# Performance work log

Hardware: AMD Instinct MI355X
Metric: run time of the kernel (lower is better)

Reference implementation:

```python
import math
import jax, jax.numpy as jnp
import numpy as np

D_MODEL = 1024
HEADS = 16
D_K = D_MODEL // HEADS
BATCH = 4
SEQ = 2048


def setup_inputs() -> dict:
    key = jax.random.key(0)
    ks = jax.random.split(key, 7)
    q = jax.random.normal(ks[0], (BATCH, SEQ, D_MODEL), dtype=jnp.float32)
    k = jax.random.normal(ks[1], (BATCH, SEQ, D_MODEL), dtype=jnp.float32)
    v = jax.random.normal(ks[2], (BATCH, SEQ, D_MODEL), dtype=jnp.float32)
    # causal mask: True = masked (filled with -inf), broadcastable over batch & heads
    mask = jnp.triu(jnp.ones((SEQ, SEQ), dtype=bool), k=1)[None, None, :, :]
    s = 1.0 / math.sqrt(D_MODEL)
    Wq = jax.random.normal(ks[3], (D_MODEL, D_MODEL), dtype=jnp.float32) * s
    Wk = jax.random.normal(ks[4], (D_MODEL, D_MODEL), dtype=jnp.float32) * s
    Wv = jax.random.normal(ks[5], (D_MODEL, D_MODEL), dtype=jnp.float32) * s
    Wo = jax.random.normal(ks[6], (D_MODEL, D_MODEL), dtype=jnp.float32) * s
    return {"q": q, "k": k, "v": v, "mask": mask, "Wq": Wq, "Wk": Wk, "Wv": Wv, "Wo": Wo}


def reference(q, k, v, mask, Wq, Wk, Wv, Wo):
    B, S, _ = q.shape
    # Linear(d_model, d_model, bias=False): y = x @ W.T
    def proj(x, W):
        return (x @ W.T).reshape(B, S, HEADS, D_K).transpose(0, 2, 1, 3)  # [B,H,S,Dk]
    qh, kh, vh = proj(q, Wq), proj(k, Wk), proj(v, Wv)
    scores = jnp.einsum('bhqd,bhkd->bhqk', qh, kh) / math.sqrt(D_K)
    scores = jnp.where(mask, -jnp.inf, scores)
    attn = jax.nn.softmax(scores, axis=-1)  # dropout p=0 is identity
    ctx = jnp.einsum('bhqk,bhkd->bhqd', attn, vh)
    ctx = ctx.transpose(0, 2, 1, 3).reshape(B, S, D_MODEL)
    return ctx @ Wo.T
```

## Files before the change

kernel.cpp:

```cpp
#include <hip/hip_runtime.h>
#include <hip/hip_bf16.h>
#include <stdint.h>

#define S_LEN 2048
#define DMODEL 1024
#define HEADS 16
#define DK 64
#define LDK 72

#define QSCALE 0.18033688011112042f

typedef __attribute__((ext_vector_type(8))) short bf16x8;
typedef __attribute__((ext_vector_type(4))) float f32x4;

__device__ __forceinline__ unsigned short f2bf(float f) {
    union { float f; unsigned u; } c; c.f = f;
    unsigned u = c.u;
    u += 0x7fffu + ((u >> 16) & 1u);
    return (unsigned short)(u >> 16);
}

__device__ __forceinline__ unsigned pkbf(float a, float b) {
    union { float f; unsigned u; } ca, cb; ca.f = a; cb.f = b;
    unsigned ua = ca.u + (0x7fffu + ((ca.u >> 16) & 1u));
    unsigned ub = cb.u + (0x7fffu + ((cb.u >> 16) & 1u));
    return __builtin_amdgcn_perm(ub, ua, 0x07060302);
}

__device__ __forceinline__ void g2lds16(const unsigned short* g, unsigned short* l) {
    __builtin_amdgcn_global_load_lds((const __attribute__((address_space(1))) void*)g,
                                     (__attribute__((address_space(3))) void*)l, 16, 0, 0);
}

__global__ __launch_bounds__(256) void convert_kernel(
    const float* __restrict__ q, const float* __restrict__ k, const float* __restrict__ v,
    const float* __restrict__ Wq, const float* __restrict__ Wk, const float* __restrict__ Wv,
    const float* __restrict__ Wo,
    unsigned short* __restrict__ qbf, unsigned short* __restrict__ kbf,
    unsigned short* __restrict__ vbf, unsigned short* __restrict__ wbf)
{
    const float* src; unsigned short* dst; int n8;
    const int y = blockIdx.y;
    if (y == 0)      { src = q;  dst = qbf;           n8 = 1048576; }
    else if (y == 1) { src = k;  dst = kbf;           n8 = 1048576; }
    else if (y == 2) { src = v;  dst = vbf;           n8 = 1048576; }
    else if (y == 3) { src = Wq; dst = wbf;           n8 = 131072; }
    else if (y == 4) { src = Wk; dst = wbf + 1048576; n8 = 131072; }
    else if (y == 5) { src = Wv; dst = wbf + 2097152; n8 = 131072; }
    else             { src = Wo; dst = wbf + 3145728; n8 = 131072; }
    int i = blockIdx.x * 256 + threadIdx.x;
    if (i >= n8) return;
    float4 f0 = ((const float4*)src)[(size_t)2 * i];
    float4 f1 = ((const float4*)src)[(size_t)2 * i + 1];
    union { unsigned u[4]; uint4 v; } o;
    o.u[0] = pkbf(f0.x, f0.y); o.u[1] = pkbf(f0.z, f0.w);
    o.u[2] = pkbf(f1.x, f1.y); o.u[3] = pkbf(f1.z, f1.w);
    *(uint4*)&dst[(size_t)8 * i] = o.v;
}

__global__ __launch_bounds__(256) void proj_gemm_kernel(
    const unsigned short* __restrict__ qbf, const unsigned short* __restrict__ kbf,
    const unsigned short* __restrict__ vbf, const unsigned short* __restrict__ wbf,
    unsigned short* __restrict__ qh, unsigned short* __restrict__ kh,
    unsigned short* __restrict__ vh_t)
{
    const unsigned short* A; const unsigned short* Bm; unsigned short* Y;
    const int z = blockIdx.z;
    if (z == 0)      { A = qbf; Bm = wbf;           Y = qh;   }
    else if (z == 1) { A = kbf; Bm = wbf + 1048576; Y = kh;   }
    else             { A = vbf; Bm = wbf + 2097152; Y = vh_t; }

    __shared__ unsigned short sA[128 * 64];
    __shared__ unsigned short sB[128 * 64];

    const int t    = threadIdx.x;
    const int lane = t & 63;
    const int wid  = t >> 6;
    const int wrow = (wid >> 1) * 64;
    const int wcol = (wid & 1) * 64;
    const int m0   = blockIdx.x * 128;
    const int n0   = blockIdx.y * 128;
    const int lrow = lane & 15;
    const int quad = lane >> 4;
    const int lk   = quad * 8;

    const unsigned short* gA = A + (size_t)(m0 + wid * 32 + (lane >> 3)) * 1024 + (lane & 7) * 8;
    const unsigned short* gB = Bm + (size_t)(n0 + wid * 32 + (lane >> 3)) * 1024 + (lane & 7) * 8;
    unsigned short* lA = sA + wid * 2048;
    unsigned short* lB = sB + wid * 2048;

    f32x4 acc[4][4];
    for (int i = 0; i < 4; i++) for (int j = 0; j < 4; j++) acc[i][j] = (f32x4){0.f, 0.f, 0.f, 0.f};

    for (int kb = 0; kb < 1024; kb += 64) {
        __syncthreads();
        for (int it = 0; it < 4; ++it) {
            g2lds16(gA + (size_t)it * 8 * 1024, lA + it * 512);
            g2lds16(gB + (size_t)it * 8 * 1024, lB + it * 512);
        }
        gA += 64; gB += 64;
        __syncthreads();
        for (int kk = 0; kk < 64; kk += 32) {
            bf16x8 a[4], b[4];
            for (int i = 0; i < 4; i++) a[i] = *(const bf16x8*)&sA[(wrow + i * 16 + lrow) * 64 + kk + lk];
            for (int j = 0; j < 4; j++) b[j] = *(const bf16x8*)&sB[(wcol + j * 16 + lrow) * 64 + kk + lk];
            for (int i = 0; i < 4; i++)
                for (int j = 0; j < 4; j++)
                    acc[i][j] = __builtin_amdgcn_mfma_f32_16x16x32_bf16(a[i], b[j], acc[i][j], 0, 0, 0);
        }
    }

    const float scale = (z == 0) ? QSCALE : 1.0f;
    for (int i = 0; i < 4; i++) {
        int grow = m0 + wrow + i * 16 + quad * 4;
        for (int j = 0; j < 4; j++) {
            int gcol = n0 + wcol + j * 16 + lrow;
            int h = gcol >> 6, d = gcol & 63;
            for (int r = 0; r < 4; r++) {
                int row = grow + r;
                int b_ = row >> 11;
                int s_ = row & 2047;
                unsigned short val = f2bf(acc[i][j][r] * scale);
                if (z == 2)
                    Y[(((size_t)(b_ * HEADS + h) * DK) + d) * S_LEN + s_] = val;
                else
                    Y[(((size_t)(b_ * HEADS + h) * S_LEN) + s_) * DK + d] = val;
            }
        }
    }
}

__global__ __launch_bounds__(256) void outproj_gemm_kernel(
    const unsigned short* __restrict__ ctx, const unsigned short* __restrict__ wobf,
    float* __restrict__ out)
{
    __shared__ unsigned short sA[128 * 64];
    __shared__ unsigned short sB[128 * 64];

    const int t    = threadIdx.x;
    const int lane = t & 63;
    const int wid  = t >> 6;
    const int wrow = (wid >> 1) * 64;
    const int wcol = (wid & 1) * 64;
    const int m0   = blockIdx.x * 128;
    const int n0   = blockIdx.y * 128;
    const int lrow = lane & 15;
    const int quad = lane >> 4;
    const int lk   = quad * 8;

    const unsigned short* gA = ctx  + (size_t)(m0 + wid * 32 + (lane >> 3)) * 1024 + (lane & 7) * 8;
    const unsigned short* gB = wobf + (size_t)(n0 + wid * 32 + (lane >> 3)) * 1024 + (lane & 7) * 8;
    unsigned short* lA = sA + wid * 2048;
    unsigned short* lB = sB + wid * 2048;

    f32x4 acc[4][4];
    for (int i = 0; i < 4; i++) for (int j = 0; j < 4; j++) acc[i][j] = (f32x4){0.f, 0.f, 0.f, 0.f};

    for (int kb = 0; kb < 1024; kb += 64) {
        __syncthreads();
        for (int it = 0; it < 4; ++it) {
            g2lds16(gA + (size_t)it * 8 * 1024, lA + it * 512);
            g2lds16(gB + (size_t)it * 8 * 1024, lB + it * 512);
        }
        gA += 64; gB += 64;
        __syncthreads();
        for (int kk = 0; kk < 64; kk += 32) {
            bf16x8 a[4], b[4];
            for (int i = 0; i < 4; i++) a[i] = *(const bf16x8*)&sA[(wrow + i * 16 + lrow) * 64 + kk + lk];
            for (int j = 0; j < 4; j++) b[j] = *(const bf16x8*)&sB[(wcol + j * 16 + lrow) * 64 + kk + lk];
            for (int i = 0; i < 4; i++)
                for (int j = 0; j < 4; j++)
                    acc[i][j] = __builtin_amdgcn_mfma_f32_16x16x32_bf16(a[i], b[j], acc[i][j], 0, 0, 0);
        }
    }

    for (int i = 0; i < 4; i++) {
        int grow = m0 + wrow + i * 16 + quad * 4;
        for (int j = 0; j < 4; j++) {
            int gcol = n0 + wcol + j * 16 + lrow;
            for (int r = 0; r < 4; r++)
                out[(size_t)(grow + r) * DMODEL + gcol] = acc[i][j][r];
        }
    }
}

__global__ __launch_bounds__(256) void attn_kernel(
    const unsigned short* __restrict__ qh, const unsigned short* __restrict__ kh,
    const unsigned short* __restrict__ vh_t, unsigned short* __restrict__ ctx)
{
    __shared__ unsigned short sK[64 * LDK];
    __shared__ unsigned short sVt[64 * LDK];
    __shared__ unsigned short sPT[4][32 * LDK];

    const int t    = threadIdx.x;
    const int lane = t & 63;
    const int wid  = t >> 6;
    const int bh   = blockIdx.y;
    const size_t base = (size_t)bh * S_LEN * DK;
    const int lrow = lane & 15;
    const int quad = lane >> 4;
    const int b_ = bh >> 4, h_ = bh & 15;
    unsigned short* myPT = &sPT[wid][0];

    for (int pass = 0; pass < 2; ++pass) {
        const int qt = pass ? (15 - (int)blockIdx.x) : (int)blockIdx.x;
        const int q0 = qt * 128;
        const int qw0 = q0 + wid * 32;

        bf16x8 qreg[2][2];
        for (int nf = 0; nf < 2; ++nf)
            for (int h = 0; h < 2; ++h)
                qreg[nf][h] = *(const bf16x8*)&qh[base + (size_t)(qw0 + nf * 16 + lrow) * DK + h * 32 + quad * 8];

        f32x4 o[4][2];
        for (int mf = 0; mf < 4; mf++) for (int nf = 0; nf < 2; nf++) o[mf][nf] = (f32x4){0.f, 0.f, 0.f, 0.f};
        float lstat[2] = { 0.f, 0.f };

        const int ntiles = q0 / 64 + 2;
        for (int kt = 0; kt < ntiles; ++kt) {
            const int k0 = kt * 64;
            __syncthreads();
            for (int it = 0; it < 2; ++it) {
                int idx = t + it * 256;
                int row = idx >> 3, c8 = (idx & 7) * 8;
                *(uint4*)&sK[row * LDK + c8]  = *(const uint4*)&kh[base + (size_t)(k0 + row) * DK + c8];
                *(uint4*)&sVt[row * LDK + c8] = *(const uint4*)&vh_t[base + (size_t)row * S_LEN + k0 + c8];
            }
            __syncthreads();

            if (k0 > qw0 + 31) continue;

            f32x4 st[4][2];
            for (int mf = 0; mf < 4; mf++) for (int nf = 0; nf < 2; nf++) st[mf][nf] = (f32x4){0.f, 0.f, 0.f, 0.f};
            for (int h = 0; h < 2; ++h) {
                bf16x8 kf[4];
                for (int mf = 0; mf < 4; mf++)
                    kf[mf] = *(const bf16x8*)&sK[(mf * 16 + lrow) * LDK + h * 32 + quad * 8];
                for (int mf = 0; mf < 4; mf++)
                    for (int nf = 0; nf < 2; nf++)
                        st[mf][nf] = __builtin_amdgcn_mfma_f32_16x16x32_bf16(kf[mf], qreg[nf][h], st[mf][nf], 0, 0, 0);
            }

            const bool need_mask = (k0 + 63 > qw0);

            for (int nf = 0; nf < 2; ++nf) {
                const int qidx = qw0 + nf * 16 + lrow;
                if (need_mask) {
                    for (int mf = 0; mf < 4; mf++)
                        for (int r = 0; r < 4; r++) {
                            int key = k0 + mf * 16 + quad * 4 + r;
                            if (key > qidx) st[mf][nf][r] = -INFINITY;
                        }
                }
                float rsum = 0.f;
                for (int mf = 0; mf < 4; mf++) {
                    float p0 = exp2f(st[mf][nf][0]);
                    float p1 = exp2f(st[mf][nf][1]);
                    float p2 = exp2f(st[mf][nf][2]);
                    float p3 = exp2f(st[mf][nf][3]);
                    rsum += (p0 + p1) + (p2 + p3);
                    uint2 pk;
                    pk.x = pkbf(p0, p1);
                    pk.y = pkbf(p2, p3);
                    *(uint2*)&myPT[(nf * 16 + lrow) * LDK + mf * 16 + quad * 4] = pk;
                }
                rsum += __shfl_xor(rsum, 16);
                rsum += __shfl_xor(rsum, 32);
                lstat[nf] += rsum;
            }

            for (int h = 0; h < 2; ++h) {
                bf16x8 vf[4], pf[2];
                for (int mf = 0; mf < 4; mf++)
                    vf[mf] = *(const bf16x8*)&sVt[(mf * 16 + lrow) * LDK + h * 32 + quad * 8];
                for (int nf = 0; nf < 2; nf++)
                    pf[nf] = *(const bf16x8*)&myPT[(nf * 16 + lrow) * LDK + h * 32 + quad * 8];
                for (int mf = 0; mf < 4; mf++)
                    for (int nf = 0; nf < 2; nf++)
                        o[mf][nf] = __builtin_amdgcn_mfma_f32_16x16x32_bf16(vf[mf], pf[nf], o[mf][nf], 0, 0, 0);
            }
        }

        for (int nf = 0; nf < 2; ++nf) {
            float inv = 1.f / lstat[nf];
            int s_ = qw0 + nf * 16 + lrow;
            size_t rowbase = (((size_t)(b_ * S_LEN + s_)) * HEADS + h_) * DK;
            for (int mf = 0; mf < 4; mf++) {
                int d0 = mf * 16 + quad * 4;
                uint2 pk;
                pk.x = pkbf(o[mf][nf][0] * inv, o[mf][nf][1] * inv);
                pk.y = pkbf(o[mf][nf][2] * inv, o[mf][nf][3] * inv);
                *(uint2*)&ctx[rowbase + d0] = pk;
            }
        }
    }
}

__global__ __launch_bounds__(256) void proj_fb_kernel(
    const float* __restrict__ q, const float* __restrict__ k, const float* __restrict__ v,
    const float* __restrict__ Wq, const float* __restrict__ Wk, const float* __restrict__ Wv,
    unsigned short* __restrict__ qh, unsigned short* __restrict__ kh, unsigned short* __restrict__ vh_t)
{
    const float* X; const float* W; unsigned short* Y;
    if (blockIdx.z == 0)      { X = q; W = Wq; Y = qh; }
    else if (blockIdx.z == 1) { X = k; W = Wk; Y = kh; }
    else                      { X = v; W = Wv; Y = vh_t; }

    __shared__ short sA[128 * LDK];
    __shared__ short sB[128 * LDK];
    const int t = threadIdx.x, lane = t & 63, wid = t >> 6;
    const int wrow = (wid >> 1) * 64, wcol = (wid & 1) * 64;
    const int m0 = blockIdx.x * 128, n0 = blockIdx.y * 128;
    const int lrow = lane & 15, quad = lane >> 4, lk = quad * 8;

    f32x4 acc[4][4];
    for (int i = 0; i < 4; i++) for (int j = 0; j < 4; j++) acc[i][j] = (f32x4){0.f, 0.f, 0.f, 0.f};

    for (int kb = 0; kb < DMODEL; kb += 64) {
        for (int it = 0; it < 8; ++it) {
            int idx = t + it * 256;
            int row = idx >> 4, c4 = (idx & 15) * 4;
            float4 fa = *(const float4*)&X[(size_t)(m0 + row) * DMODEL + kb + c4];
            float4 fb = *(const float4*)&W[(size_t)(n0 + row) * DMODEL + kb + c4];
            short4 sa = { (short)f2bf(fa.x), (short)f2bf(fa.y), (short)f2bf(fa.z), (short)f2bf(fa.w) };
            short4 sb = { (short)f2bf(fb.x), (short)f2bf(fb.y), (short)f2bf(fb.z), (short)f2bf(fb.w) };
            *(short4*)&sA[row * LDK + c4] = sa;
            *(short4*)&sB[row * LDK + c4] = sb;
        }
        __syncthreads();
        for (int kk = 0; kk < 64; kk += 32) {
            bf16x8 a[4], b[4];
            for (int i = 0; i < 4; i++) a[i] = *(const bf16x8*)&sA[(wrow + i * 16 + lrow) * LDK + kk + lk];
            for (int j = 0; j < 4; j++) b[j] = *(const bf16x8*)&sB[(wcol + j * 16 + lrow) * LDK + kk + lk];
            for (int i = 0; i < 4; i++)
                for (int j = 0; j < 4; j++)
                    acc[i][j] = __builtin_amdgcn_mfma_f32_16x16x32_bf16(a[i], b[j], acc[i][j], 0, 0, 0);
        }
        __syncthreads();
    }

    const float scale = (blockIdx.z == 0) ? QSCALE : 1.0f;
    for (int i = 0; i < 4; i++) {
        int grow = m0 + wrow + i * 16 + quad * 4;
        for (int j = 0; j < 4; j++) {
            int gcol = n0 + wcol + j * 16 + lrow;
            int h = gcol >> 6, d = gcol & 63;
            for (int r = 0; r < 4; r++) {
                int row = grow + r, b_ = row >> 11, s_ = row & 2047;
                unsigned short val = f2bf(acc[i][j][r] * scale);
                if (blockIdx.z == 2)
                    Y[(((size_t)(b_ * HEADS + h) * DK) + d) * S_LEN + s_] = val;
                else
                    Y[(((size_t)(b_ * HEADS + h) * S_LEN) + s_) * DK + d] = val;
            }
        }
    }
}

__global__ __launch_bounds__(256) void outproj_fb_kernel(
    const unsigned short* __restrict__ ctx, const float* __restrict__ Wo, float* __restrict__ out)
{
    __shared__ short sA[128 * LDK];
    __shared__ short sB[128 * LDK];
    const int t = threadIdx.x, lane = t & 63, wid = t >> 6;
    const int wrow = (wid >> 1) * 64, wcol = (wid & 1) * 64;
    const int m0 = blockIdx.x * 128, n0 = blockIdx.y * 128;
    const int lrow = lane & 15, quad = lane >> 4, lk = quad * 8;

    f32x4 acc[4][4];
    for (int i = 0; i < 4; i++) for (int j = 0; j < 4; j++) acc[i][j] = (f32x4){0.f, 0.f, 0.f, 0.f};

    for (int kb = 0; kb < DMODEL; kb += 64) {
        for (int it = 0; it < 4; ++it) {
            int idx = t + it * 256;
            int row = idx >> 3, c8 = (idx & 7) * 8;
            *(uint4*)&sA[row * LDK + c8] = *(const uint4*)&ctx[(size_t)(m0 + row) * DMODEL + kb + c8];
        }
        for (int it = 0; it < 8; ++it) {
            int idx = t + it * 256;
            int row = idx >> 4, c4 = (idx & 15) * 4;
            float4 fb = *(const float4*)&Wo[(size_t)(n0 + row) * DMODEL + kb + c4];
            short4 sb = { (short)f2bf(fb.x), (short)f2bf(fb.y), (short)f2bf(fb.z), (short)f2bf(fb.w) };
            *(short4*)&sB[row * LDK + c4] = sb;
        }
        __syncthreads();
        for (int kk = 0; kk < 64; kk += 32) {
            bf16x8 a[4], b[4];
            for (int i = 0; i < 4; i++) a[i] = *(const bf16x8*)&sA[(wrow + i * 16 + lrow) * LDK + kk + lk];
            for (int j = 0; j < 4; j++) b[j] = *(const bf16x8*)&sB[(wcol + j * 16 + lrow) * LDK + kk + lk];
            for (int i = 0; i < 4; i++)
                for (int j = 0; j < 4; j++)
                    acc[i][j] = __builtin_amdgcn_mfma_f32_16x16x32_bf16(a[i], b[j], acc[i][j], 0, 0, 0);
        }
        __syncthreads();
    }

    for (int i = 0; i < 4; i++) {
        int grow = m0 + wrow + i * 16 + quad * 4;
        for (int j = 0; j < 4; j++) {
            int gcol = n0 + wcol + j * 16 + lrow;
            for (int r = 0; r < 4; r++)
                out[(size_t)(grow + r) * DMODEL + gcol] = acc[i][j][r];
        }
    }
}

extern "C" void kernel_launch(void* const* d_in, const int* in_sizes, int n_in,
                              void* d_out, int out_size, void* d_ws, size_t ws_size,
                              hipStream_t stream)
{
    const float* q  = (const float*)d_in[0];
    const float* k  = (const float*)d_in[1];
    const float* v  = (const float*)d_in[2];
    const float* Wq = (const float*)d_in[4];
    const float* Wk = (const float*)d_in[5];
    const float* Wv = (const float*)d_in[6];
    const float* Wo = (const float*)d_in[7];
    float* out = (float*)d_out;

    const size_t M8 = (size_t)8 * 1024 * 1024;
    const size_t need = (size_t)(52) * 1024 * 1024 * 2;

    if (ws_size >= need) {
        unsigned short* qbf  = (unsigned short*)d_ws;
        unsigned short* kbf  = qbf + M8;
        unsigned short* vbf  = kbf + M8;
        unsigned short* wbf  = vbf + M8;
        unsigned short* qh   = wbf + (size_t)4 * 1024 * 1024;
        unsigned short* kh   = qh + M8;
        unsigned short* vh_t = kh + M8;
        unsigned short* ctx  = qbf;

        dim3 gCvt(4096, 7);
        convert_kernel<<<gCvt, 256, 0, stream>>>(q, k, v, Wq, Wk, Wv, Wo, qbf, kbf, vbf, wbf);

        dim3 gProj(64, 8, 3);
        proj_gemm_kernel<<<gProj, 256, 0, stream>>>(qbf, kbf, vbf, wbf, qh, kh, vh_t);

        dim3 gAttn(8, 64);
        attn_kernel<<<gAttn, 256, 0, stream>>>(qh, kh, vh_t, ctx);

        dim3 gOut(64, 8);
        outproj_gemm_kernel<<<gOut, 256, 0, stream>>>(ctx, wbf + (size_t)3 * 1024 * 1024, out);
    } else {
        unsigned short* qh   = (unsigned short*)d_ws;
        unsigned short* kh   = qh + M8;
        unsigned short* vh_t = kh + M8;
        unsigned short* ctx  = vh_t + M8;

        dim3 gProj(64, 8, 3);
        proj_fb_kernel<<<gProj, 256, 0, stream>>>(q, k, v, Wq, Wk, Wv, qh, kh, vh_t);

        dim3 gAttn(8, 64);
        attn_kernel<<<gAttn, 256, 0, stream>>>(qh, kh, vh_t, ctx);

        dim3 gOut(64, 8);
        outproj_fb_kernel<<<gOut, 256, 0, stream>>>(ctx, Wo, out);
    }
}
```

Baseline: 358.3 us.

## Register-prefetch next K/V tile, remap blocks, defer row-sum reduction in attention

The attention kernel now loads the next K and V^T tile into registers while the current tile is being computed, so global load latency overlaps with the MFMA work. Block indices are remapped so that consecutive workgroups spread across batch-heads, which changes how work lands on XCDs and their caches. The per-tile cross-lane row-sum shuffles are deferred to a single reduction at the end, fp32-to-bf16 packing uses the hardware v_cvt_pk_bf16_f32 instruction, and the MFMA sections are wrapped in s_setprio. The cost is extra registers for the prefetch buffers, which may reduce occupancy.

```diff
diff --git a/kernel.cpp b/kernel.cpp
--- a/kernel.cpp
+++ b/kernel.cpp
@@ -25,6 +25,12 @@
     unsigned ua = ca.u + (0x7fffu + ((ca.u >> 16) & 1u));
     unsigned ub = cb.u + (0x7fffu + ((cb.u >> 16) & 1u));
     return __builtin_amdgcn_perm(ub, ua, 0x07060302);
+}
+
+__device__ __forceinline__ unsigned cvtpk(float a, float b) {
+    unsigned r;
+    asm("v_cvt_pk_bf16_f32 %0, %1, %2" : "=v"(r) : "v"(a), "v"(b));
+    return r;
 }
 
 __device__ __forceinline__ void g2lds16(const unsigned short* g, unsigned short* l) {
@@ -195,15 +201,23 @@
     const int t    = threadIdx.x;
     const int lane = t & 63;
     const int wid  = t >> 6;
-    const int bh   = blockIdx.y;
+    const int lin  = (int)(blockIdx.y * gridDim.x + blockIdx.x);
+    const int wlin = (lin & 7) * 64 + (lin >> 3);
+    const int qx   = wlin & 7;
+    const int bh   = wlin >> 3;
     const size_t base = (size_t)bh * S_LEN * DK;
     const int lrow = lane & 15;
     const int quad = lane >> 4;
     const int b_ = bh >> 4, h_ = bh & 15;
     unsigned short* myPT = &sPT[wid][0];
 
+    const int sr0 = t >> 3;
+    const int sc0 = (t & 7) * 8;
+    const unsigned short* gK = kh + base;
+    const unsigned short* gV = vh_t + base;
+
     for (int pass = 0; pass < 2; ++pass) {
-        const int qt = pass ? (15 - (int)blockIdx.x) : (int)blockIdx.x;
+        const int qt = pass ? (15 - qx) : qx;
         const int q0 = qt * 128;
         const int qw0 = q0 + wid * 32;
 
@@ -217,14 +231,25 @@
         float lstat[2] = { 0.f, 0.f };
 
         const int ntiles = q0 / 64 + 2;
+
+        uint4 rK0 = *(const uint4*)&gK[(size_t)sr0 * DK + sc0];
+        uint4 rK1 = *(const uint4*)&gK[(size_t)(sr0 + 32) * DK + sc0];
+        uint4 rV0 = *(const uint4*)&gV[(size_t)sr0 * S_LEN + sc0];
+        uint4 rV1 = *(const uint4*)&gV[(size_t)(sr0 + 32) * S_LEN + sc0];
+
         for (int kt = 0; kt < ntiles; ++kt) {
             const int k0 = kt * 64;
             __syncthreads();
-            for (int it = 0; it < 2; ++it) {
-                int idx = t + it * 256;
-                int row = idx >> 3, c8 = (idx & 7) * 8;
-                *(uint4*)&sK[row * LDK + c8]  = *(const uint4*)&kh[base + (size_t)(k0 + row) * DK + c8];
-                *(uint4*)&sVt[row * LDK + c8] = *(const uint4*)&vh_t[base + (size_t)row * S_LEN + k0 + c8];
+            *(uint4*)&sK [sr0 * LDK + sc0]        = rK0;
+            *(uint4*)&sK [(sr0 + 32) * LDK + sc0] = rK1;
+            *(uint4*)&sVt[sr0 * LDK + sc0]        = rV0;
+            *(uint4*)&sVt[(sr0 + 32) * LDK + sc0] = rV1;
+            if (kt + 1 < ntiles) {
+                const int kn = k0 + 64;
+                rK0 = *(const uint4*)&gK[(size_t)(kn + sr0) * DK + sc0];
+                rK1 = *(const uint4*)&gK[(size_t)(kn + sr0 + 32) * DK + sc0];
+                rV0 = *(const uint4*)&gV[(size_t)sr0 * S_LEN + kn + sc0];
+                rV1 = *(const uint4*)&gV[(size_t)(sr0 + 32) * S_LEN + kn + sc0];
             }
             __syncthreads();
 
@@ -236,9 +261,11 @@
                 bf16x8 kf[4];
                 for (int mf = 0; mf < 4; mf++)
                     kf[mf] = *(const bf16x8*)&sK[(mf * 16 + lrow) * LDK + h * 32 + quad * 8];
+                __builtin_amdgcn_s_setprio(1);
                 for (int mf = 0; mf < 4; mf++)
                     for (int nf = 0; nf < 2; nf++)
                         st[mf][nf] = __builtin_amdgcn_mfma_f32_16x16x32_bf16(kf[mf], qreg[nf][h], st[mf][nf], 0, 0, 0);
+                __builtin_amdgcn_s_setprio(0);
             }
 
             const bool need_mask = (k0 + 63 > qw0);
@@ -260,12 +287,10 @@
                     float p3 = exp2f(st[mf][nf][3]);
                     rsum += (p0 + p1) + (p2 + p3);
                     uint2 pk;
-                    pk.x = pkbf(p0, p1);
-                    pk.y = pkbf(p2, p3);
+                    pk.x = cvtpk(p0, p1);
+                    pk.y = cvtpk(p2, p3);
                     *(uint2*)&myPT[(nf * 16 + lrow) * LDK + mf * 16 + quad * 4] = pk;
                 }
-                rsum += __shfl_xor(rsum, 16);
-                rsum += __shfl_xor(rsum, 32);
                 lstat[nf] += rsum;
             }
 
@@ -275,14 +300,19 @@
                     vf[mf] = *(const bf16x8*)&sVt[(mf * 16 + lrow) * LDK + h * 32 + quad * 8];
                 for (int nf = 0; nf < 2; nf++)
                     pf[nf] = *(const bf16x8*)&myPT[(nf * 16 + lrow) * LDK + h * 32 + quad * 8];
+                __builtin_amdgcn_s_setprio(1);
                 for (int mf = 0; mf < 4; mf++)
                     for (int nf = 0; nf < 2; nf++)
                         o[mf][nf] = __builtin_amdgcn_mfma_f32_16x16x32_bf16(vf[mf], pf[nf], o[mf][nf], 0, 0, 0);
+                __builtin_amdgcn_s_setprio(0);
             }
         }
 
         for (int nf = 0; nf < 2; ++nf) {
-            float inv = 1.f / lstat[nf];
+            float ls = lstat[nf];
+            ls += __shfl_xor(ls, 16);
+            ls += __shfl_xor(ls, 32);
+            float inv = 1.f / ls;
             int s_ = qw0 + nf * 16 + lrow;
             size_t rowbase = (((size_t)(b_ * S_LEN + s_)) * HEADS + h_) * DK;
             for (int mf = 0; mf < 4; mf++) {
```

After: 344.7 us. 1.04x faster.
